# Performance work log

Measured on AMD Instinct MI355X. Metric: run time of the kernel, lower is better.

Reference implementation:

```python
import jax, jax.numpy as jnp
import numpy as np

B, D_IN, EMB = 8192, 4000, 96
H0, H1 = 2048, 1024
NB, NC, OPT = 8, 8, 32
NE = NB * NC  # 64 experts (total contests)


def setup_inputs() -> dict:
    key = jax.random.key(0)
    ks = jax.random.split(key, 10)
    scale = lambda fan_in: jnp.sqrt(2.0 / fan_in)  # kaiming_normal-ish
    return {
        "inputs": jax.random.normal(ks[0], (B, D_IN), dtype=jnp.float32),
        "emb_table": jax.random.normal(ks[1], (NE, EMB), dtype=jnp.float32) * scale(EMB),
        "W0": jax.random.normal(ks[2], (D_IN + EMB, H0), dtype=jnp.float32) * scale(D_IN + EMB),
        "b0": jnp.zeros((H0,), dtype=jnp.float32),
        "W1": jax.random.normal(ks[3], (H0, H1), dtype=jnp.float32) * scale(H0),
        "b1": jnp.zeros((H1,), dtype=jnp.float32),
        "We": jax.random.normal(ks[4], (NE, H1, OPT), dtype=jnp.float32) * scale(H1),
        "be": jnp.zeros((NE, OPT), dtype=jnp.float32),
        "ballot_number": jax.random.randint(ks[5], (B,), 0, NB, dtype=jnp.int32),
        "contest_number": jax.random.randint(ks[6], (B,), 0, NC, dtype=jnp.int32),
        "batches": B,
    }


def reference(inputs, emb_table, W0, b0, W1, b1, We, be,
              ballot_number, contest_number, batches):
    # flat expert index per sample: index_of[ballot][contest] with equal-size ballots
    expert = ballot_number * NC + contest_number                  # [B]
    x = inputs.reshape(batches, -1)                               # [B, D_IN]
    emb = emb_table[expert]                                       # [B, EMB] (gather)
    h = jnp.concatenate([emb, x], axis=1)                         # [B, D_IN+EMB]
    h = jax.nn.relu(h @ W0 + b0)                                  # fc0 (dropout = id at eval)
    h = jax.nn.relu(h @ W1 + b1)                                  # fc1
    # per-sample routed linear: gather expert weights, batched matvec
    out = jnp.einsum("bd,bdo->bo", h, We[expert]) + be[expert]    # [B, OPT]
    return jax.nn.sigmoid(out)
```

## Files before the change

kernel.cpp:

```cpp
#include <hip/hip_runtime.h>
#include <math.h>

typedef __attribute__((ext_vector_type(8))) short short8;
typedef __attribute__((ext_vector_type(4))) float f32x4;

#define B_SZ 8192
#define D_INN 4000
#define EMBD 96
#define H0D 2048
#define H1D 1024
#define KDIM 4096

__device__ __forceinline__ unsigned short f2bf(float f) {
  union { float f; unsigned u; } v; v.f = f;
  unsigned r = v.u + 0x7FFFu + ((v.u >> 16) & 1u);
  return (unsigned short)(r >> 16);
}
__device__ __forceinline__ float bf2f(unsigned short h) {
  union { unsigned u; float f; } v; v.u = ((unsigned)h) << 16;
  return v.f;
}
__device__ __forceinline__ void gld_lds16(const void* g, void* l) {
  __builtin_amdgcn_global_load_lds(
      (const __attribute__((address_space(1))) unsigned int*)g,
      (__attribute__((address_space(3))) unsigned int*)l, 16, 0, 0);
}

__global__ __launch_bounds__(256) void transpose_cvt(
    const float* __restrict__ in, unsigned short* __restrict__ out, int R, int C) {
  __shared__ float tile[32][33];
  int c0 = blockIdx.x * 32, r0 = blockIdx.y * 32;
  int tc = threadIdx.x & 31, tr = threadIdx.x >> 5;
#pragma unroll
  for (int i = 0; i < 4; ++i) {
    int r = tr + i * 8;
    tile[r][tc] = in[(size_t)(r0 + r) * C + (c0 + tc)];
  }
  __syncthreads();
#pragma unroll
  for (int i = 0; i < 4; ++i) {
    int rr = tr + i * 8;
    out[(size_t)(c0 + rr) * R + (r0 + tc)] = f2bf(tile[tc][rr]);
  }
}

__global__ __launch_bounds__(256) void build_A(
    const float* __restrict__ inputs, const float* __restrict__ emb,
    const int* __restrict__ ballot, const int* __restrict__ contest,
    unsigned short* __restrict__ A) {
  int gid = blockIdx.x * 256 + threadIdx.x;
  int b = gid >> 9, c = gid & 511;
  const float* src;
  if (c < EMBD / 8) {
    int e = ballot[b] * 8 + contest[b];
    src = emb + (size_t)e * EMBD + c * 8;
  } else {
    src = inputs + (size_t)b * D_INN + (c - EMBD / 8) * 8;
  }
  float4 v0 = *(const float4*)src;
  float4 v1 = *(const float4*)(src + 4);
  unsigned short r[8];
  r[0] = f2bf(v0.x); r[1] = f2bf(v0.y); r[2] = f2bf(v0.z); r[3] = f2bf(v0.w);
  r[4] = f2bf(v1.x); r[5] = f2bf(v1.y); r[6] = f2bf(v1.z); r[7] = f2bf(v1.w);
  *reinterpret_cast<short8*>(A + (size_t)b * KDIM + c * 8) =
      *reinterpret_cast<const short8*>(r);
}

template <int MREP>
__global__ __launch_bounds__(512, 2) void gemm_nt_pipe(
    const unsigned short* __restrict__ A, const unsigned short* __restrict__ Bt,
    const float* __restrict__ bias, unsigned short* __restrict__ C,
    int K, int N, int NBN) {
  constexpr int BM  = MREP * 32;
  constexpr int AI  = MREP / 4;
  constexpr int ASH = MREP * 1024;
  constexpr int NLD = AI + 2;
  __shared__ unsigned short lds[3 * ASH + 3 * 8192];

  const int tid = threadIdx.x;
  const int w = tid >> 6, l = tid & 63;
  const int lr = l & 15, kg = l >> 4;
  const int wm = w >> 2, wn = w & 3;

  int swz = (blockIdx.x & 7) * ((int)gridDim.x >> 3) + ((int)blockIdx.x >> 3);
  const int bm = swz / NBN, bn = swz - bm * NBN;
  const int NT = K >> 5;

  const int rg = l >> 2;
  const int sl = ((l & 3) ^ ((l >> 3) & 3)) * 8;
  const unsigned short* ga[AI];
#pragma unroll
  for (int i = 0; i < AI; ++i)
    ga[i] = A + (size_t)(bm * BM + (i * 8 + w) * 16 + rg) * K + sl;
  const unsigned short* gb[2];
#pragma unroll
  for (int j = 0; j < 2; ++j)
    gb[j] = Bt + (size_t)(bn * 256 + (j * 8 + w) * 16 + rg) * K + sl;

  const int xo = (kg ^ ((lr >> 1) & 3)) << 4;
  const int aoff = (wm * (MREP * 16) + lr) * 64 + xo;
  const int boff = (wn * 64 + lr) * 64 + xo;

  f32x4 acc[MREP][4] = {};

  auto stage = [&](int t, int rbuf) {
    unsigned short* la = lds + rbuf * ASH + w * 512;
    unsigned short* lb = lds + 3 * ASH + rbuf * 8192 + w * 512;
    const int ko = t * 32;
#pragma unroll
    for (int i = 0; i < AI; ++i) gld_lds16(ga[i] + ko, la + i * 4096);
    gld_lds16(gb[0] + ko, lb);
    gld_lds16(gb[1] + ko, lb + 4096);
  };

  stage(0, 0);
  stage(1, 1);
  if constexpr (NLD == 4) asm volatile("s_waitcnt vmcnt(4)" ::: "memory");
  else                    asm volatile("s_waitcnt vmcnt(3)" ::: "memory");
  __builtin_amdgcn_s_barrier();
  __builtin_amdgcn_sched_barrier(0);

  int rb = 0;
  for (int t = 0; t < NT; ++t) {
    int rb2 = rb + 2; if (rb2 >= 3) rb2 -= 3;
    if (t + 2 < NT) stage(t + 2, rb2);

    const char* pa = (const char*)lds + rb * (ASH * 2) + aoff;
    const char* pb = (const char*)lds + 6 * ASH + rb * 16384 + boff;
    short8 a[MREP], b[4];
#pragma unroll
    for (int mi = 0; mi < MREP; ++mi) a[mi] = *(const short8*)(pa + mi * 1024);
#pragma unroll
    for (int ni = 0; ni < 4; ++ni)   b[ni] = *(const short8*)(pb + ni * 1024);

    __builtin_amdgcn_s_setprio(1);
#pragma unroll
    for (int mi = 0; mi < MREP; ++mi)
#pragma unroll
      for (int ni = 0; ni < 4; ++ni)
        acc[mi][ni] = __builtin_amdgcn_mfma_f32_16x16x32_bf16(
            a[mi], b[ni], acc[mi][ni], 0, 0, 0);
    __builtin_amdgcn_s_setprio(0);

    __builtin_amdgcn_sched_barrier(0);
    asm volatile("s_waitcnt lgkmcnt(0)" ::: "memory");
    if (t + 2 < NT) {
      if constexpr (NLD == 4) asm volatile("s_waitcnt vmcnt(4)" ::: "memory");
      else                    asm volatile("s_waitcnt vmcnt(3)" ::: "memory");
      __builtin_amdgcn_s_barrier();
    } else if (t + 1 < NT) {
      asm volatile("s_waitcnt vmcnt(0)" ::: "memory");
      __builtin_amdgcn_s_barrier();
    }
    __builtin_amdgcn_sched_barrier(0);

    rb = rb + 1; if (rb >= 3) rb = 0;
  }

#pragma unroll
  for (int mi = 0; mi < MREP; ++mi) {
    const int row0 = bm * BM + wm * (MREP * 16) + mi * 16 + kg * 4;
#pragma unroll
    for (int ni = 0; ni < 4; ++ni) {
      const int col = bn * 256 + wn * 64 + ni * 16 + lr;
      const float bv = bias[col];
#pragma unroll
      for (int j = 0; j < 4; ++j) {
        float v = acc[mi][ni][j] + bv;
        v = v > 0.f ? v : 0.f;
        C[(size_t)(row0 + j) * N + col] = f2bf(v);
      }
    }
  }
}

__global__ __launch_bounds__(256) void expert_head(
    const unsigned short* __restrict__ h1, const float* __restrict__ We,
    const float* __restrict__ be, const int* __restrict__ ballot,
    const int* __restrict__ contest, float* __restrict__ out) {
  int b = blockIdx.x * 4 + (threadIdx.x >> 6);
  int lane = threadIdx.x & 63;
  int o = lane & 31, half = lane >> 5;
  int e = ballot[b] * 8 + contest[b];
  const unsigned short* hrow = h1 + (size_t)b * H1D + half * 512;
  const float* wb = We + ((size_t)e * H1D + half * 512) * 32 + o;
  float acc = 0.f;
  for (int d0 = 0; d0 < 512; d0 += 8) {
    short8 hv = *reinterpret_cast<const short8*>(&hrow[d0]);
#pragma unroll
    for (int j = 0; j < 8; ++j)
      acc = fmaf(bf2f((unsigned short)hv[j]), wb[(size_t)(d0 + j) * 32], acc);
  }
  acc += __shfl_xor(acc, 32, 64);
  if (half == 0) {
    float x = acc + be[e * 32 + o];
    out[(size_t)b * 32 + o] = 1.f / (1.f + expf(-x));
  }
}

extern "C" void kernel_launch(void* const* d_in, const int* in_sizes, int n_in,
                              void* d_out, int out_size, void* d_ws, size_t ws_size,
                              hipStream_t stream) {
  const float* inputs = (const float*)d_in[0];
  const float* emb    = (const float*)d_in[1];
  const float* W0     = (const float*)d_in[2];
  const float* b0     = (const float*)d_in[3];
  const float* W1     = (const float*)d_in[4];
  const float* b1     = (const float*)d_in[5];
  const float* We     = (const float*)d_in[6];
  const float* be     = (const float*)d_in[7];
  const int* ballot   = (const int*)d_in[8];
  const int* contest  = (const int*)d_in[9];
  float* out = (float*)d_out;

  char* ws = (char*)d_ws;
  unsigned short* A   = (unsigned short*)(ws);
  unsigned short* W0t = (unsigned short*)(ws + 67108864);
  unsigned short* h0  = (unsigned short*)(ws + 83886080);
  unsigned short* W1t = (unsigned short*)(ws + 117440512);
  unsigned short* h1  = (unsigned short*)(ws + 121634816);

  dim3 blk(256);
  transpose_cvt<<<dim3(H0D / 32, KDIM / 32, 1), blk, 0, stream>>>(W0, W0t, KDIM, H0D);
  transpose_cvt<<<dim3(H1D / 32, H0D / 32, 1), blk, 0, stream>>>(W1, W1t, H0D, H1D);
  build_A<<<dim3(B_SZ * 512 / 256), blk, 0, stream>>>(inputs, emb, ballot, contest, A);
  gemm_nt_pipe<8><<<dim3((B_SZ / 256) * (H0D / 256)), dim3(512), 0, stream>>>(
      A, W0t, b0, h0, KDIM, H0D, H0D / 256);
  gemm_nt_pipe<4><<<dim3((B_SZ / 128) * (H1D / 256)), dim3(512), 0, stream>>>(
      h0, W1t, b1, h1, H0D, H1D, H1D / 256);
  expert_head<<<dim3(B_SZ / 4), blk, 0, stream>>>(h1, We, be, ballot, contest, out);
}
```

Before: 265.2 us.

## Split GEMM k-step into two MFMA halves interleaved with staged A/B loads

Restructures the GEMM main loop so each k-tile's MFMA work is split into two halves over the M fragments. The A prefetch is issued between the first LDS reads and the first half, and the B prefetch between the second-half LDS reads and the second half, with a barrier placed in each half. The aim is to spread global-to-LDS traffic and LDS reads across the MFMA work so the matrix units stall less. It adds an extra barrier per iteration and depends on the vmcnt accounting staying correct with the split stage ordering. The sched_barrier fences are also removed, which lets the compiler reorder the code around the new structure.

```diff
diff --git a/kernel.cpp b/kernel.cpp
--- a/kernel.cpp
+++ b/kernel.cpp
@@ -73,8 +73,8 @@
     int K, int N, int NBN) {
   constexpr int BM  = MREP * 32;
   constexpr int AI  = MREP / 4;
-  constexpr int ASH = MREP * 1024;
-  constexpr int NLD = AI + 2;
+  constexpr int ASH = BM * 32;
+  constexpr int MH  = MREP / 2;
   __shared__ unsigned short lds[3 * ASH + 3 * 8192];
 
   const int tid = threadIdx.x;
@@ -92,10 +92,8 @@
 #pragma unroll
   for (int i = 0; i < AI; ++i)
     ga[i] = A + (size_t)(bm * BM + (i * 8 + w) * 16 + rg) * K + sl;
-  const unsigned short* gb[2];
-#pragma unroll
-  for (int j = 0; j < 2; ++j)
-    gb[j] = Bt + (size_t)(bn * 256 + (j * 8 + w) * 16 + rg) * K + sl;
+  const unsigned short* gb0 = Bt + (size_t)(bn * 256 + w * 16 + rg) * K + sl;
+  const unsigned short* gb1 = gb0 + (size_t)128 * K;
 
   const int xo = (kg ^ ((lr >> 1) & 3)) << 4;
   const int aoff = (wm * (MREP * 16) + lr) * 64 + xo;
@@ -103,56 +101,75 @@
 
   f32x4 acc[MREP][4] = {};
 
-  auto stage = [&](int t, int rbuf) {
+  auto stageA = [&](int t, int rbuf) {
     unsigned short* la = lds + rbuf * ASH + w * 512;
+    const int ko = t * 32;
+#pragma unroll
+    for (int i = 0; i < AI; ++i) gld_lds16(ga[i] + ko, la + i * 4096);
+  };
+  auto stageB = [&](int t, int rbuf) {
     unsigned short* lb = lds + 3 * ASH + rbuf * 8192 + w * 512;
     const int ko = t * 32;
-#pragma unroll
-    for (int i = 0; i < AI; ++i) gld_lds16(ga[i] + ko, la + i * 4096);
-    gld_lds16(gb[0] + ko, lb);
-    gld_lds16(gb[1] + ko, lb + 4096);
+    gld_lds16(gb0 + ko, lb);
+    gld_lds16(gb1 + ko, lb + 4096);
   };
 
-  stage(0, 0);
-  stage(1, 1);
-  if constexpr (NLD == 4) asm volatile("s_waitcnt vmcnt(4)" ::: "memory");
-  else                    asm volatile("s_waitcnt vmcnt(3)" ::: "memory");
+#define WAIT_VM_STEADY() do { \
+    if constexpr (AI == 2) asm volatile("s_waitcnt vmcnt(4)" ::: "memory"); \
+    else                   asm volatile("s_waitcnt vmcnt(3)" ::: "memory"); \
+  } while (0)
+
+  stageA(0, 0); stageB(0, 0);
+  stageA(1, 1); stageB(1, 1);
+  WAIT_VM_STEADY();
   __builtin_amdgcn_s_barrier();
-  __builtin_amdgcn_sched_barrier(0);
 
   int rb = 0;
   for (int t = 0; t < NT; ++t) {
     int rb2 = rb + 2; if (rb2 >= 3) rb2 -= 3;
-    if (t + 2 < NT) stage(t + 2, rb2);
-
     const char* pa = (const char*)lds + rb * (ASH * 2) + aoff;
-    const char* pb = (const char*)lds + 6 * ASH + rb * 16384 + boff;
-    short8 a[MREP], b[4];
-#pragma unroll
-    for (int mi = 0; mi < MREP; ++mi) a[mi] = *(const short8*)(pa + mi * 1024);
-#pragma unroll
-    for (int ni = 0; ni < 4; ++ni)   b[ni] = *(const short8*)(pb + ni * 1024);
-
+    const char* pb = (const char*)lds + 3 * (ASH * 2) + rb * 16384 + boff;
+
+    short8 a0[MH], bfr[4];
+#pragma unroll
+    for (int mi = 0; mi < MH; ++mi) a0[mi] = *(const short8*)(pa + mi * 1024);
+#pragma unroll
+    for (int ni = 0; ni < 4; ++ni)  bfr[ni] = *(const short8*)(pb + ni * 1024);
+    if (t + 2 < NT) stageA(t + 2, rb2);
+    asm volatile("s_waitcnt lgkmcnt(0)" ::: "memory");
+    __builtin_amdgcn_s_barrier();
     __builtin_amdgcn_s_setprio(1);
 #pragma unroll
-    for (int mi = 0; mi < MREP; ++mi)
+    for (int mi = 0; mi < MH; ++mi)
 #pragma unroll
       for (int ni = 0; ni < 4; ++ni)
         acc[mi][ni] = __builtin_amdgcn_mfma_f32_16x16x32_bf16(
-            a[mi], b[ni], acc[mi][ni], 0, 0, 0);
+            a0[mi], bfr[ni], acc[mi][ni], 0, 0, 0);
     __builtin_amdgcn_s_setprio(0);
 
-    __builtin_amdgcn_sched_barrier(0);
-    asm volatile("s_waitcnt lgkmcnt(0)" ::: "memory");
+    short8 a1[MH];
+#pragma unroll
+    for (int mi = 0; mi < MH; ++mi) a1[mi] = *(const short8*)(pa + (MH + mi) * 1024);
     if (t + 2 < NT) {
-      if constexpr (NLD == 4) asm volatile("s_waitcnt vmcnt(4)" ::: "memory");
-      else                    asm volatile("s_waitcnt vmcnt(3)" ::: "memory");
+      stageB(t + 2, rb2);
+      asm volatile("s_waitcnt lgkmcnt(0)" ::: "memory");
+      WAIT_VM_STEADY();
       __builtin_amdgcn_s_barrier();
     } else if (t + 1 < NT) {
+      asm volatile("s_waitcnt lgkmcnt(0)" ::: "memory");
       asm volatile("s_waitcnt vmcnt(0)" ::: "memory");
       __builtin_amdgcn_s_barrier();
+    } else {
+      asm volatile("s_waitcnt lgkmcnt(0)" ::: "memory");
     }
-    __builtin_amdgcn_sched_barrier(0);
+    __builtin_amdgcn_s_setprio(1);
+#pragma unroll
+    for (int mi = 0; mi < MH; ++mi)
+#pragma unroll
+      for (int ni = 0; ni < 4; ++ni)
+        acc[MH + mi][ni] = __builtin_amdgcn_mfma_f32_16x16x32_bf16(
+            a1[mi], bfr[ni], acc[MH + mi][ni], 0, 0, 0);
+    __builtin_amdgcn_s_setprio(0);
 
     rb = rb + 1; if (rb >= 3) rb = 0;
   }
@@ -172,6 +189,7 @@
       }
     }
   }
+#undef WAIT_VM_STEADY
 }
 
 __global__ __launch_bounds__(256) void expert_head(
```

Result: no change. 264.3 us (-0.3%).
